# Optimization experiments

Hardware: AMD Instinct MI355X
Metric: run time of the kernel (lower is better)

Reference implementation:

```python
import jax, jax.numpy as jnp
import numpy as np

E = 64          # num_experts
TOPK = 8        # num_experts_per_tok
I = 512         # moe_intermediate_size
H = 1024        # hidden_size
G = 128         # awq group_size
T = 2048        # tokens (batch*seq)

# AWQ nibble unpack order: bit shifts [0,16,4,20,8,24,12,28] -> indices [0,4,1,5,2,6,3,7]
_AWQ_SHIFTS = jnp.array([0, 4, 1, 5, 2, 6, 3, 7], dtype=jnp.int32) * 4


def awq_dequant(qw, qz, scales, group_size=G):
    """qw: (K, N//8) int32, qz: (K//G, N//8) int32, scales: (K//G, N) float.
    Returns dense weight (K, N): (q - z) * scale with per-group zero/scale."""
    K = qw.shape[0]
    uq = ((qw[:, :, None] >> _AWQ_SHIFTS) & 0xF).reshape(K, -1)          # (K, N)
    uz = ((qz[:, :, None] >> _AWQ_SHIFTS) & 0xF).reshape(qz.shape[0], -1)  # (K//G, N)
    uz = jnp.repeat(uz, group_size, axis=0)                               # (K, N)
    sc = jnp.repeat(scales, group_size, axis=0)                           # (K, N)
    return (uq.astype(scales.dtype) - uz.astype(scales.dtype)) * sc


def setup_inputs() -> dict:
    key = jax.random.key(0)
    ks = jax.random.split(key, 8)
    imax = 2**31 - 1
    return {
        "x": jax.random.normal(ks[0], (T, H), dtype=jnp.float32),
        "gate_w": jax.random.normal(ks[1], (E, H), dtype=jnp.float32) * 0.02,
        "qweight1": jax.random.randint(ks[2], (H, (E * I) // 8), 0, imax, dtype=jnp.int32),
        "qzeros1": jax.random.randint(ks[3], (H // G, (E * I) // 8), 0, imax, dtype=jnp.int32),
        "scales1": jax.random.normal(ks[4], (H // G, E * I), dtype=jnp.float32) * 0.02,
        "qweight2": jax.random.randint(ks[5], (I, (E * H) // 8), 0, imax, dtype=jnp.int32),
        "qzeros2": jax.random.randint(ks[6], (I // G, (E * H) // 8), 0, imax, dtype=jnp.int32),
        "scales2": jax.random.normal(ks[7], (I // G, E * H), dtype=jnp.float32) * 0.02,
    }


def reference(x, gate_w, qweight1, qzeros1, scales1, qweight2, qzeros2, scales2):
    # dequant grouped expert weights
    w1 = awq_dequant(qweight1, qzeros1, scales1).T.reshape(E, I, H)   # (E, I, H)
    w2 = awq_dequant(qweight2, qzeros2, scales2).T.reshape(E, H, I)   # (E, H, I)

    # routing: softmax -> top-k -> renormalize
    logits = x @ gate_w.T                                             # (T, E)
    probs = jax.nn.softmax(logits, axis=-1)
    topv, topi = jax.lax.top_k(probs, TOPK)                           # (T, K)
    topv = topv / jnp.sum(topv, axis=-1, keepdims=True)
    cw = jnp.sum(jax.nn.one_hot(topi, E, dtype=x.dtype) * topv[..., None], axis=1)  # (T, E)

    # experts: out = sum_e cw[t,e] * silu(x @ w1[e].T) @ w2[e].T
    h = jax.nn.silu(jnp.einsum('th,eih->tei', x, w1))                 # (T, E, I)
    h = h * cw[:, :, None]                                            # fold combine weights
    out = jnp.einsum('tei,ehi->th', h, w2)                            # (T, H)
    return out
```

## Files before the change

kernel.cpp:

```cpp
#include <hip/hip_runtime.h>
#include <hip/hip_bf16.h>

#define T_TOK 2048
#define HID   1024
#define EXP   64
#define TOPK  8
#define IMED  512
#define N1 (EXP * IMED)
#define C1 (N1 / 8)
#define N2 (EXP * HID)
#define C2 (N2 / 8)

typedef __bf16 bf16x8 __attribute__((ext_vector_type(8)));
typedef float f32x4 __attribute__((ext_vector_type(4)));
typedef unsigned short ushortx8 __attribute__((ext_vector_type(8)));
typedef unsigned short ushortx4 __attribute__((ext_vector_type(4)));

__constant__ int kShifts[8] = {0, 16, 4, 20, 8, 24, 12, 28};

__device__ __forceinline__ void async16(const void* g, void* l) {
  __builtin_amdgcn_global_load_lds((const __attribute__((address_space(1))) void*)g,
                                   (__attribute__((address_space(3))) void*)l, 16, 0, 0);
}

__device__ __forceinline__ unsigned short f2bf(float f) {
  unsigned u = __builtin_bit_cast(unsigned, f);
  unsigned r = (u + 0x7fffu + ((u >> 16) & 1u)) >> 16;
  return (unsigned short)r;
}

__device__ __forceinline__ float bf2f(unsigned short b) {
  unsigned u = ((unsigned)b) << 16;
  return __builtin_bit_cast(float, u);
}

__device__ __forceinline__ bf16x8 unpack8(unsigned q, float s, float w) {
  bf16x8 r;
#pragma unroll
  for (int i = 0; i < 8; ++i) {
    const float qf = (float)((q >> (4 * i)) & 15u);
    r[i] = (__bf16)fmaf(qf, s, w);
  }
  return r;
}

__global__ __launch_bounds__(256) void routing_kernel(
    const float* __restrict__ x, const float* __restrict__ gate_w,
    int* __restrict__ counts, int* __restrict__ tok_list,
    int* __restrict__ hslot_list, float* __restrict__ cw_list,
    unsigned short* __restrict__ xbf) {
  const int t = blockIdx.x;
  const int tid = threadIdx.x;
  __shared__ float xs[HID];
  __shared__ float part[64][4];

  float4 v = reinterpret_cast<const float4*>(x + (size_t)t * HID)[tid];
  reinterpret_cast<float4*>(xs)[tid] = v;
  ushortx4 o;
  o[0] = f2bf(v.x); o[1] = f2bf(v.y); o[2] = f2bf(v.z); o[3] = f2bf(v.w);
  *reinterpret_cast<ushortx4*>(xbf + (size_t)t * HID + tid * 4) = o;
  __syncthreads();

  const int e = tid >> 2, seg = tid & 3;
  const float4* gp = reinterpret_cast<const float4*>(gate_w + (size_t)e * HID);
  const float4* xp = reinterpret_cast<const float4*>(xs);
  float acc = 0.f;
#pragma unroll 8
  for (int i = 0; i < 64; ++i) {
    float4 a = xp[i * 4 + seg];
    float4 b = gp[i * 4 + seg];
    acc = fmaf(a.x, b.x, acc);
    acc = fmaf(a.y, b.y, acc);
    acc = fmaf(a.z, b.z, acc);
    acc = fmaf(a.w, b.w, acc);
  }
  part[e][seg] = acc;
  __syncthreads();

  if (tid < 64) {
    float4 p = reinterpret_cast<const float4*>(part)[tid];
    float lg = (p.x + p.y) + (p.z + p.w);

    float m = lg;
    for (int off = 32; off; off >>= 1) m = fmaxf(m, __shfl_xor(m, off));
    float pe = expf(lg - m);
    float s = pe;
    for (int off = 32; off; off >>= 1) s += __shfl_xor(s, off);
    float prob = pe / s;

    float pcur = prob;
    float myv = 0.f;
    int myi = -1;
    float tsum = 0.f;
    for (int k = 0; k < TOPK; ++k) {
      float vv = pcur;
      int idx = tid;
      for (int off = 32; off; off >>= 1) {
        float ov = __shfl_xor(vv, off);
        int oi = __shfl_xor(idx, off);
        if (ov > vv || (ov == vv && oi < idx)) { vv = ov; idx = oi; }
      }
      tsum += vv;
      if (tid == k) { myv = vv; myi = idx; }
      if (tid == idx) pcur = -1.f;
    }

    if (tid < TOPK) {
      float cw = myv / tsum;
      int ex = myi;
      int slot = atomicAdd(&counts[ex], 1);
      tok_list[ex * T_TOK + slot] = t;
      hslot_list[ex * T_TOK + slot] = t * TOPK + tid;
      cw_list[ex * T_TOK + slot] = cw;
    }
  }
}

__global__ __launch_bounds__(256) void repack_kernel(
    const int* __restrict__ qw, unsigned* __restrict__ qk, int K, int C) {
  const int kd = blockIdx.y;
  const int c = blockIdx.x * 512 + threadIdx.x * 2;
  unsigned q[8][2];
#pragma unroll
  for (int r = 0; r < 8; ++r) {
    const int2 v = *reinterpret_cast<const int2*>(qw + (size_t)(kd * 8 + r) * C + c);
    q[r][0] = (unsigned)v.x;
    q[r][1] = (unsigned)v.y;
  }
  unsigned outd[16];
#pragma unroll
  for (int ci = 0; ci < 2; ++ci) {
#pragma unroll
    for (int jj = 0; jj < 8; ++jj) {
      const int sh = kShifts[jj];
      unsigned o = 0;
#pragma unroll
      for (int r = 0; r < 8; ++r) o |= ((q[r][ci] >> sh) & 0xFu) << (4 * r);
      outd[ci * 8 + jj] = o;
    }
  }
  unsigned* dst = qk + ((size_t)(c >> 1) * (K / 8) + kd) * 16;
#pragma unroll
  for (int i = 0; i < 4; ++i)
    *reinterpret_cast<uint4*>(dst + i * 4) = *reinterpret_cast<const uint4*>(&outd[i * 4]);
}

__global__ __launch_bounds__(256) void mfma_gemm1(
    const unsigned short* __restrict__ xbf, const unsigned* __restrict__ qk1,
    const int* __restrict__ qz1, const float* __restrict__ sc1,
    const int* __restrict__ counts, const int* __restrict__ tok_list,
    const int* __restrict__ hslot_list, const float* __restrict__ cw_list,
    unsigned short* __restrict__ h_buf) {
  const int e = blockIdx.z;
  const int n_e = counts[e];
  const int t0 = blockIdx.y * 64;
  if (t0 >= n_e) return;
  const int ntile = blockIdx.x;
  const int tid = threadIdx.x;
  const int wave = tid >> 6, lane = tid & 63;
  const int wm = wave & 1, wn = wave >> 1;
  const int fr = lane & 15, fq = lane >> 4;

  __shared__ unsigned short As[2][64 * 64];

  const int arow = tid >> 3;
  const int acb = ((tid & 7) ^ ((tid >> 3) & 7)) * 16;
  const int ta0 = tok_list[e * T_TOK + min(t0 + arow, n_e - 1)];
  const int ta1 = tok_list[e * T_TOK + min(t0 + 32 + arow, n_e - 1)];
  const char* ga0 = (const char*)(xbf + (size_t)ta0 * HID) + acb;
  const char* ga1 = (const char*)(xbf + (size_t)ta1 * HID) + acb;

  auto stage = [&](int b) {
    char* l = (char*)&As[b][0] + wave * 1024;
    async16(ga0, l);
    async16(ga1, l + 4096);
    ga0 += 128; ga1 += 128;
  };

  const int nbase = e * IMED + ntile * 64 + wn * 32;
  const unsigned* bl0 = qk1 + (size_t)(nbase >> 4) * 2048 + fq * 16 + fr;
  const unsigned* bl1 = bl0 + 2048;
  const int shz = ((fr >> 1) & 3) * 4 + (fr & 1) * 16;

  f32x4 acc[2][2];
#pragma unroll
  for (int i = 0; i < 2; ++i)
#pragma unroll
    for (int j = 0; j < 2; ++j) acc[i][j] = (f32x4){0.f, 0.f, 0.f, 0.f};

  stage(0);
  unsigned cb00 = bl0[0], cb01 = bl0[64], cb10 = bl1[0], cb11 = bl1[64];
  int p = 0;
#pragma unroll 1
  for (int g = 0; g < HID / 128; ++g) {
    const float s0f = sc1[(size_t)g * N1 + nbase + fr];
    const float s1f = sc1[(size_t)g * N1 + nbase + 16 + fr];
    const unsigned zd0 = (unsigned)qz1[(size_t)g * C1 + (nbase >> 3) + (fr >> 3)];
    const unsigned zd1 = (unsigned)qz1[(size_t)g * C1 + 2 + (nbase >> 3) + (fr >> 3)];
    const float w0f = -(float)((zd0 >> shz) & 15u) * s0f;
    const float w1f = -(float)((zd1 >> shz) & 15u) * s1f;
#pragma unroll
    for (int hh = 0; hh < 2; ++hh) {
      const int k0 = g * 128 + hh * 64;
      __syncthreads();
      if (k0 + 64 < HID) stage(p ^ 1);
      unsigned nb00 = 0, nb01 = 0, nb10 = 0, nb11 = 0;
      if (k0 + 64 < HID) {
        const unsigned* q0 = bl0 + (k0 + 64) * 2;
        const unsigned* q1 = bl1 + (k0 + 64) * 2;
        nb00 = q0[0]; nb01 = q0[64]; nb10 = q1[0]; nb11 = q1[64];
      }
      const bf16x8 b00 = unpack8(cb00, s0f, w0f);
      const bf16x8 b01 = unpack8(cb01, s0f, w0f);
      const bf16x8 b10 = unpack8(cb10, s1f, w1f);
      const bf16x8 b11 = unpack8(cb11, s1f, w1f);
#pragma unroll
      for (int kk = 0; kk < 2; ++kk) {
        bf16x8 af[2];
#pragma unroll
        for (int i = 0; i < 2; ++i) {
          const int row = wm * 32 + i * 16 + fr;
          af[i] = *reinterpret_cast<const bf16x8*>(
              &As[p][row * 64 + (((kk * 4 + fq) ^ (fr & 7)) * 8)]);
        }
        const bf16x8 b0 = kk ? b01 : b00;
        const bf16x8 b1 = kk ? b11 : b10;
        acc[0][0] = __builtin_amdgcn_mfma_f32_16x16x32_bf16(af[0], b0, acc[0][0], 0, 0, 0);
        acc[0][1] = __builtin_amdgcn_mfma_f32_16x16x32_bf16(af[0], b1, acc[0][1], 0, 0, 0);
        acc[1][0] = __builtin_amdgcn_mfma_f32_16x16x32_bf16(af[1], b0, acc[1][0], 0, 0, 0);
        acc[1][1] = __builtin_amdgcn_mfma_f32_16x16x32_bf16(af[1], b1, acc[1][1], 0, 0, 0);
      }
      cb00 = nb00; cb01 = nb01; cb10 = nb10; cb11 = nb11;
      p ^= 1;
    }
  }

#pragma unroll
  for (int i = 0; i < 2; ++i) {
#pragma unroll
    for (int r = 0; r < 4; ++r) {
      const int grow = t0 + wm * 32 + i * 16 + fq * 4 + r;
      if (grow < n_e) {
        const float cw = cw_list[e * T_TOK + grow];
        const int hs = hslot_list[e * T_TOK + grow];
        unsigned short* dst = h_buf + (size_t)hs * IMED + ntile * 64 + wn * 32 + fr;
#pragma unroll
        for (int j = 0; j < 2; ++j) {
          const float v = acc[i][j][r];
          dst[j * 16] = f2bf((v / (1.f + expf(-v))) * cw);
        }
      }
    }
  }
}

__global__ __launch_bounds__(256) void mfma_gemm2(
    const unsigned short* __restrict__ h_buf, const unsigned* __restrict__ qk2,
    const int* __restrict__ qz2, const float* __restrict__ sc2,
    const int* __restrict__ counts, const int* __restrict__ hslot_list,
    unsigned short* __restrict__ p_buf) {
  const int e = blockIdx.z;
  const int n_e = counts[e];
  const int t0 = blockIdx.y * 64;
  if (t0 >= n_e) return;
  const int ntile = blockIdx.x;
  const int tid = threadIdx.x;
  const int wave = tid >> 6, lane = tid & 63;
  const int wm = wave & 1, wn = wave >> 1;
  const int fr = lane & 15, fq = lane >> 4;

  __shared__ unsigned short As[2][64 * 64];

  const int arow = tid >> 3;
  const int acb = ((tid & 7) ^ ((tid >> 3) & 7)) * 16;
  const int ha0 = hslot_list[e * T_TOK + min(t0 + arow, n_e - 1)];
  const int ha1 = hslot_list[e * T_TOK + min(t0 + 32 + arow, n_e - 1)];
  const char* ga0 = (const char*)(h_buf + (size_t)ha0 * IMED) + acb;
  const char* ga1 = (const char*)(h_buf + (size_t)ha1 * IMED) + acb;

  auto stage = [&](int b) {
    char* l = (char*)&As[b][0] + wave * 1024;
    async16(ga0, l);
    async16(ga1, l + 4096);
    ga0 += 128; ga1 += 128;
  };

  const int nbase = e * HID + ntile * 64 + wn * 32;
  const unsigned* bl0 = qk2 + (size_t)(nbase >> 4) * 1024 + fq * 16 + fr;
  const unsigned* bl1 = bl0 + 1024;
  const int shz = ((fr >> 1) & 3) * 4 + (fr & 1) * 16;

  f32x4 acc[2][2];
#pragma unroll
  for (int i = 0; i < 2; ++i)
#pragma unroll
    for (int j = 0; j < 2; ++j) acc[i][j] = (f32x4){0.f, 0.f, 0.f, 0.f};

  stage(0);
  unsigned cb00 = bl0[0], cb01 = bl0[64], cb10 = bl1[0], cb11 = bl1[64];
  int p = 0;
#pragma unroll 1
  for (int g = 0; g < IMED / 128; ++g) {
    const float s0f = sc2[(size_t)g * N2 + nbase + fr];
    const float s1f = sc2[(size_t)g * N2 + nbase + 16 + fr];
    const unsigned zd0 = (unsigned)qz2[(size_t)g * C2 + (nbase >> 3) + (fr >> 3)];
    const unsigned zd1 = (unsigned)qz2[(size_t)g * C2 + 2 + (nbase >> 3) + (fr >> 3)];
    const float w0f = -(float)((zd0 >> shz) & 15u) * s0f;
    const float w1f = -(float)((zd1 >> shz) & 15u) * s1f;
#pragma unroll
    for (int hh = 0; hh < 2; ++hh) {
      const int k0 = g * 128 + hh * 64;
      __syncthreads();
      if (k0 + 64 < IMED) stage(p ^ 1);
      unsigned nb00 = 0, nb01 = 0, nb10 = 0, nb11 = 0;
      if (k0 + 64 < IMED) {
        const unsigned* q0 = bl0 + (k0 + 64) * 2;
        const unsigned* q1 = bl1 + (k0 + 64) * 2;
        nb00 = q0[0]; nb01 = q0[64]; nb10 = q1[0]; nb11 = q1[64];
      }
      const bf16x8 b00 = unpack8(cb00, s0f, w0f);
      const bf16x8 b01 = unpack8(cb01, s0f, w0f);
      const bf16x8 b10 = unpack8(cb10, s1f, w1f);
      const bf16x8 b11 = unpack8(cb11, s1f, w1f);
#pragma unroll
      for (int kk = 0; kk < 2; ++kk) {
        bf16x8 af[2];
#pragma unroll
        for (int i = 0; i < 2; ++i) {
          const int row = wm * 32 + i * 16 + fr;
          af[i] = *reinterpret_cast<const bf16x8*>(
              &As[p][row * 64 + (((kk * 4 + fq) ^ (fr & 7)) * 8)]);
        }
        const bf16x8 b0 = kk ? b01 : b00;
        const bf16x8 b1 = kk ? b11 : b10;
        acc[0][0] = __builtin_amdgcn_mfma_f32_16x16x32_bf16(af[0], b0, acc[0][0], 0, 0, 0);
        acc[0][1] = __builtin_amdgcn_mfma_f32_16x16x32_bf16(af[0], b1, acc[0][1], 0, 0, 0);
        acc[1][0] = __builtin_amdgcn_mfma_f32_16x16x32_bf16(af[1], b0, acc[1][0], 0, 0, 0);
        acc[1][1] = __builtin_amdgcn_mfma_f32_16x16x32_bf16(af[1], b1, acc[1][1], 0, 0, 0);
      }
      cb00 = nb00; cb01 = nb01; cb10 = nb10; cb11 = nb11;
      p ^= 1;
    }
  }

#pragma unroll
  for (int i = 0; i < 2; ++i) {
#pragma unroll
    for (int r = 0; r < 4; ++r) {
      const int grow = t0 + wm * 32 + i * 16 + fq * 4 + r;
      if (grow < n_e) {
        const int hs = hslot_list[e * T_TOK + grow];
        unsigned short* dst = p_buf + (size_t)hs * HID + ntile * 64 + wn * 32 + fr;
#pragma unroll
        for (int j = 0; j < 2; ++j) dst[j * 16] = f2bf(acc[i][j][r]);
      }
    }
  }
}

__global__ __launch_bounds__(256) void reduce_kernel(const unsigned short* __restrict__ p_buf,
                                                     float* __restrict__ out) {
  const int idx = blockIdx.x * 256 + threadIdx.x;
  const int t = idx >> 7;
  const int c0 = (idx & 127) * 8;
  float s[8] = {0.f, 0.f, 0.f, 0.f, 0.f, 0.f, 0.f, 0.f};
#pragma unroll
  for (int k = 0; k < TOPK; ++k) {
    ushortx8 v = *reinterpret_cast<const ushortx8*>(p_buf + ((size_t)t * TOPK + k) * HID + c0);
#pragma unroll
    for (int j = 0; j < 8; ++j) s[j] += bf2f(v[j]);
  }
  float* dst = out + (size_t)t * HID + c0;
  *reinterpret_cast<float4*>(dst) = make_float4(s[0], s[1], s[2], s[3]);
  *reinterpret_cast<float4*>(dst + 4) = make_float4(s[4], s[5], s[6], s[7]);
}

extern "C" void kernel_launch(void* const* d_in, const int* in_sizes, int n_in,
                              void* d_out, int out_size, void* d_ws, size_t ws_size,
                              hipStream_t stream) {
  const float* x      = (const float*)d_in[0];
  const float* gate_w = (const float*)d_in[1];
  const int*   qw1    = (const int*)d_in[2];
  const int*   qz1    = (const int*)d_in[3];
  const float* sc1    = (const float*)d_in[4];
  const int*   qw2    = (const int*)d_in[5];
  const int*   qz2    = (const int*)d_in[6];
  const float* sc2    = (const float*)d_in[7];
  float* out = (float*)d_out;

  char* ws = (char*)d_ws;
  int* counts           = (int*)(ws);
  int* tok_list         = (int*)(ws + 256);
  int* hslot_list       = (int*)(ws + 524544);
  float* cw_list        = (float*)(ws + 1048832);
  unsigned short* h_buf = (unsigned short*)(ws + 1573120);
  unsigned short* xbf   = (unsigned short*)(ws + 18350336);
  unsigned* qk1         = (unsigned*)(ws + 22544640);
  unsigned* qk2         = (unsigned*)(ws + 39321856);
  unsigned short* p_buf = (unsigned short*)(ws + 56099072);

  hipMemsetAsync(counts, 0, 256, stream);

  routing_kernel<<<T_TOK, 256, 0, stream>>>(x, gate_w, counts, tok_list, hslot_list, cw_list, xbf);
  repack_kernel<<<dim3(C1 / 512, HID / 8), 256, 0, stream>>>(qw1, qk1, HID, C1);
  repack_kernel<<<dim3(C2 / 512, IMED / 8), 256, 0, stream>>>(qw2, qk2, IMED, C2);

  mfma_gemm1<<<dim3(IMED / 64, T_TOK / 64, EXP), 256, 0, stream>>>(
      xbf, qk1, qz1, sc1, counts, tok_list, hslot_list, cw_list, h_buf);
  mfma_gemm2<<<dim3(HID / 64, T_TOK / 64, EXP), 256, 0, stream>>>(
      h_buf, qk2, qz2, sc2, counts, hslot_list, p_buf);
  reduce_kernel<<<(T_TOK * HID / 8) / 256, 256, 0, stream>>>(p_buf, out);
}
```

Measured before the change: 292.2 us.

## Switch expert GEMMs to fp16 with magic-number dequant and 16-column wave tiles

Converts activations, intermediate buffers and MFMA ops from bf16 to fp16, so int4 weights can be dequantized with the 0x6400 magic-number trick and packed half2 subtract/multiply instead of per-element float conversion and FMA. The repack kernel now writes a layout where each lane loads a contiguous uint2 per k-step. Each wave owns 16 output columns across all 64 rows instead of a 32x32 quadrant. Scale and zero loads are prefetched one group ahead. Fp16 has a narrower range than bf16, which risks overflow or precision differences, and the new wave tiling trades fewer dequant ops per wave for more LDS A-fragment reads.

```diff
diff --git a/kernel.cpp b/kernel.cpp
--- a/kernel.cpp
+++ b/kernel.cpp
@@ -11,10 +11,11 @@
 #define N2 (EXP * HID)
 #define C2 (N2 / 8)
 
-typedef __bf16 bf16x8 __attribute__((ext_vector_type(8)));
+typedef _Float16 h16x2 __attribute__((ext_vector_type(2)));
+typedef _Float16 h16x8 __attribute__((ext_vector_type(8)));
 typedef float f32x4 __attribute__((ext_vector_type(4)));
+typedef unsigned short ushortx4 __attribute__((ext_vector_type(4)));
 typedef unsigned short ushortx8 __attribute__((ext_vector_type(8)));
-typedef unsigned short ushortx4 __attribute__((ext_vector_type(4)));
 
 __constant__ int kShifts[8] = {0, 16, 4, 20, 8, 24, 12, 28};
 
@@ -23,32 +24,30 @@
                                    (__attribute__((address_space(3))) void*)l, 16, 0, 0);
 }
 
-__device__ __forceinline__ unsigned short f2bf(float f) {
-  unsigned u = __builtin_bit_cast(unsigned, f);
-  unsigned r = (u + 0x7fffu + ((u >> 16) & 1u)) >> 16;
-  return (unsigned short)r;
-}
-
-__device__ __forceinline__ float bf2f(unsigned short b) {
-  unsigned u = ((unsigned)b) << 16;
-  return __builtin_bit_cast(float, u);
-}
-
-__device__ __forceinline__ bf16x8 unpack8(unsigned q, float s, float w) {
-  bf16x8 r;
-#pragma unroll
-  for (int i = 0; i < 8; ++i) {
-    const float qf = (float)((q >> (4 * i)) & 15u);
-    r[i] = (__bf16)fmaf(qf, s, w);
-  }
-  return r;
+__device__ __forceinline__ unsigned short f2h(float f) {
+  return __builtin_bit_cast(unsigned short, (_Float16)f);
+}
+__device__ __forceinline__ float h2f(unsigned short b) {
+  return (float)__builtin_bit_cast(_Float16, b);
+}
+
+__device__ __forceinline__ h16x8 unpack8h(unsigned q, h16x2 sh2, h16x2 zh2) {
+  union { unsigned u[4]; h16x8 v; } out;
+#pragma unroll
+  for (int j = 0; j < 4; ++j) {
+    const unsigned m = ((q >> (4 * j)) & 0x000F000Fu) | 0x64006400u;
+    h16x2 d = __builtin_bit_cast(h16x2, m) - zh2;
+    d = d * sh2;
+    out.u[j] = __builtin_bit_cast(unsigned, d);
+  }
+  return out.v;
 }
 
 __global__ __launch_bounds__(256) void routing_kernel(
     const float* __restrict__ x, const float* __restrict__ gate_w,
     int* __restrict__ counts, int* __restrict__ tok_list,
     int* __restrict__ hslot_list, float* __restrict__ cw_list,
-    unsigned short* __restrict__ xbf) {
+    unsigned short* __restrict__ xh) {
   const int t = blockIdx.x;
   const int tid = threadIdx.x;
   __shared__ float xs[HID];
@@ -57,8 +56,8 @@
   float4 v = reinterpret_cast<const float4*>(x + (size_t)t * HID)[tid];
   reinterpret_cast<float4*>(xs)[tid] = v;
   ushortx4 o;
-  o[0] = f2bf(v.x); o[1] = f2bf(v.y); o[2] = f2bf(v.z); o[3] = f2bf(v.w);
-  *reinterpret_cast<ushortx4*>(xbf + (size_t)t * HID + tid * 4) = o;
+  o[0] = f2h(v.x); o[1] = f2h(v.y); o[2] = f2h(v.z); o[3] = f2h(v.w);
+  *reinterpret_cast<ushortx4*>(xh + (size_t)t * HID + tid * 4) = o;
   __syncthreads();
 
   const int e = tid >> 2, seg = tid & 3;
@@ -118,35 +117,40 @@
 
 __global__ __launch_bounds__(256) void repack_kernel(
     const int* __restrict__ qw, unsigned* __restrict__ qk, int K, int C) {
-  const int kd = blockIdx.y;
-  const int c = blockIdx.x * 512 + threadIdx.x * 2;
-  unsigned q[8][2];
+  const int pp = blockIdx.y;
+  const int t = pp >> 2, fq = pp & 3;
+  const int c2 = blockIdx.x * 512 + threadIdx.x * 2;
+  const int nblk = c2 >> 1;
+  unsigned o0[16], o1[16];
+#pragma unroll
+  for (int i = 0; i < 16; ++i) { o0[i] = 0u; o1[i] = 0u; }
+  const int k0a = t * 64 + fq * 8;
+  const int k0b = t * 64 + (fq + 4) * 8;
 #pragma unroll
   for (int r = 0; r < 8; ++r) {
-    const int2 v = *reinterpret_cast<const int2*>(qw + (size_t)(kd * 8 + r) * C + c);
-    q[r][0] = (unsigned)v.x;
-    q[r][1] = (unsigned)v.y;
-  }
-  unsigned outd[16];
-#pragma unroll
-  for (int ci = 0; ci < 2; ++ci) {
-#pragma unroll
-    for (int jj = 0; jj < 8; ++jj) {
-      const int sh = kShifts[jj];
-      unsigned o = 0;
-#pragma unroll
-      for (int r = 0; r < 8; ++r) o |= ((q[r][ci] >> sh) & 0xFu) << (4 * r);
-      outd[ci * 8 + jj] = o;
-    }
-  }
-  unsigned* dst = qk + ((size_t)(c >> 1) * (K / 8) + kd) * 16;
-#pragma unroll
-  for (int i = 0; i < 4; ++i)
-    *reinterpret_cast<uint4*>(dst + i * 4) = *reinterpret_cast<const uint4*>(&outd[i * 4]);
+    const int2 va = *reinterpret_cast<const int2*>(qw + (size_t)(k0a + r) * C + c2);
+    const int2 vb = *reinterpret_cast<const int2*>(qw + (size_t)(k0b + r) * C + c2);
+    const int outsh = (r & 1) * 16 + (r >> 1) * 4;
+    const unsigned qa[2] = {(unsigned)va.x, (unsigned)va.y};
+    const unsigned qb[2] = {(unsigned)vb.x, (unsigned)vb.y};
+#pragma unroll
+    for (int ci = 0; ci < 2; ++ci) {
+#pragma unroll
+      for (int j = 0; j < 8; ++j) {
+        const int sh = kShifts[j];
+        o0[ci * 8 + j] |= ((qa[ci] >> sh) & 0xFu) << outsh;
+        o1[ci * 8 + j] |= ((qb[ci] >> sh) & 0xFu) << outsh;
+      }
+    }
+  }
+  unsigned* dst = qk + (size_t)nblk * 2 * K + t * 128 + fq * 32;
+#pragma unroll
+  for (int idx = 0; idx < 16; ++idx)
+    *reinterpret_cast<uint2*>(dst + idx * 2) = make_uint2(o0[idx], o1[idx]);
 }
 
 __global__ __launch_bounds__(256) void mfma_gemm1(
-    const unsigned short* __restrict__ xbf, const unsigned* __restrict__ qk1,
+    const unsigned short* __restrict__ xh, const unsigned* __restrict__ qk1,
     const int* __restrict__ qz1, const float* __restrict__ sc1,
     const int* __restrict__ counts, const int* __restrict__ tok_list,
     const int* __restrict__ hslot_list, const float* __restrict__ cw_list,
@@ -158,7 +162,6 @@
   const int ntile = blockIdx.x;
   const int tid = threadIdx.x;
   const int wave = tid >> 6, lane = tid & 63;
-  const int wm = wave & 1, wn = wave >> 1;
   const int fr = lane & 15, fq = lane >> 4;
 
   __shared__ unsigned short As[2][64 * 64];
@@ -167,8 +170,8 @@
   const int acb = ((tid & 7) ^ ((tid >> 3) & 7)) * 16;
   const int ta0 = tok_list[e * T_TOK + min(t0 + arow, n_e - 1)];
   const int ta1 = tok_list[e * T_TOK + min(t0 + 32 + arow, n_e - 1)];
-  const char* ga0 = (const char*)(xbf + (size_t)ta0 * HID) + acb;
-  const char* ga1 = (const char*)(xbf + (size_t)ta1 * HID) + acb;
+  const char* ga0 = (const char*)(xh + (size_t)ta0 * HID) + acb;
+  const char* ga1 = (const char*)(xh + (size_t)ta1 * HID) + acb;
 
   auto stage = [&](int b) {
     char* l = (char*)&As[b][0] + wave * 1024;
@@ -177,78 +180,67 @@
     ga0 += 128; ga1 += 128;
   };
 
-  const int nbase = e * IMED + ntile * 64 + wn * 32;
-  const unsigned* bl0 = qk1 + (size_t)(nbase >> 4) * 2048 + fq * 16 + fr;
-  const unsigned* bl1 = bl0 + 2048;
+  const int nbase = e * IMED + ntile * 64 + wave * 16;
+  const unsigned* bp = qk1 + (size_t)(nbase >> 4) * (2 * HID) + fq * 32 + fr * 2;
+  const int col = nbase + fr;
   const int shz = ((fr >> 1) & 3) * 4 + (fr & 1) * 16;
 
-  f32x4 acc[2][2];
-#pragma unroll
-  for (int i = 0; i < 2; ++i)
-#pragma unroll
-    for (int j = 0; j < 2; ++j) acc[i][j] = (f32x4){0.f, 0.f, 0.f, 0.f};
+  f32x4 acc[4];
+#pragma unroll
+  for (int i = 0; i < 4; ++i) acc[i] = (f32x4){0.f, 0.f, 0.f, 0.f};
 
   stage(0);
-  unsigned cb00 = bl0[0], cb01 = bl0[64], cb10 = bl1[0], cb11 = bl1[64];
+  uint2 qcur = *reinterpret_cast<const uint2*>(bp);
+  float s_cur = sc1[col];
+  unsigned zd_cur = (unsigned)qz1[col >> 3];
   int p = 0;
 #pragma unroll 1
   for (int g = 0; g < HID / 128; ++g) {
-    const float s0f = sc1[(size_t)g * N1 + nbase + fr];
-    const float s1f = sc1[(size_t)g * N1 + nbase + 16 + fr];
-    const unsigned zd0 = (unsigned)qz1[(size_t)g * C1 + (nbase >> 3) + (fr >> 3)];
-    const unsigned zd1 = (unsigned)qz1[(size_t)g * C1 + 2 + (nbase >> 3) + (fr >> 3)];
-    const float w0f = -(float)((zd0 >> shz) & 15u) * s0f;
-    const float w1f = -(float)((zd1 >> shz) & 15u) * s1f;
+    const unsigned shb = (unsigned)f2h(s_cur);
+    const h16x2 sh2 = __builtin_bit_cast(h16x2, shb | (shb << 16));
+    const unsigned zb = 0x6400u | ((zd_cur >> shz) & 15u);
+    const h16x2 zh2 = __builtin_bit_cast(h16x2, zb | (zb << 16));
+    float s_nxt = 0.f; unsigned zd_nxt = 0u;
 #pragma unroll
     for (int hh = 0; hh < 2; ++hh) {
-      const int k0 = g * 128 + hh * 64;
+      const int t = g * 2 + hh;
       __syncthreads();
-      if (k0 + 64 < HID) stage(p ^ 1);
-      unsigned nb00 = 0, nb01 = 0, nb10 = 0, nb11 = 0;
-      if (k0 + 64 < HID) {
-        const unsigned* q0 = bl0 + (k0 + 64) * 2;
-        const unsigned* q1 = bl1 + (k0 + 64) * 2;
-        nb00 = q0[0]; nb01 = q0[64]; nb10 = q1[0]; nb11 = q1[64];
-      }
-      const bf16x8 b00 = unpack8(cb00, s0f, w0f);
-      const bf16x8 b01 = unpack8(cb01, s0f, w0f);
-      const bf16x8 b10 = unpack8(cb10, s1f, w1f);
-      const bf16x8 b11 = unpack8(cb11, s1f, w1f);
+      if (t + 1 < HID / 64) stage(p ^ 1);
+      uint2 qnext = make_uint2(0u, 0u);
+      if (t + 1 < HID / 64) qnext = *reinterpret_cast<const uint2*>(bp + (t + 1) * 128);
+      if (hh == 1 && g + 1 < HID / 128) {
+        s_nxt = sc1[(size_t)(g + 1) * N1 + col];
+        zd_nxt = (unsigned)qz1[(size_t)(g + 1) * C1 + (col >> 3)];
+      }
+      const h16x8 b0 = unpack8h(qcur.x, sh2, zh2);
+      const h16x8 b1 = unpack8h(qcur.y, sh2, zh2);
 #pragma unroll
       for (int kk = 0; kk < 2; ++kk) {
-        bf16x8 af[2];
-#pragma unroll
-        for (int i = 0; i < 2; ++i) {
-          const int row = wm * 32 + i * 16 + fr;
-          af[i] = *reinterpret_cast<const bf16x8*>(
+        const h16x8 bb = kk ? b1 : b0;
+#pragma unroll
+        for (int i = 0; i < 4; ++i) {
+          const int row = i * 16 + fr;
+          const h16x8 a = *reinterpret_cast<const h16x8*>(
               &As[p][row * 64 + (((kk * 4 + fq) ^ (fr & 7)) * 8)]);
+          acc[i] = __builtin_amdgcn_mfma_f32_16x16x32_f16(a, bb, acc[i], 0, 0, 0);
         }
-        const bf16x8 b0 = kk ? b01 : b00;
-        const bf16x8 b1 = kk ? b11 : b10;
-        acc[0][0] = __builtin_amdgcn_mfma_f32_16x16x32_bf16(af[0], b0, acc[0][0], 0, 0, 0);
-        acc[0][1] = __builtin_amdgcn_mfma_f32_16x16x32_bf16(af[0], b1, acc[0][1], 0, 0, 0);
-        acc[1][0] = __builtin_amdgcn_mfma_f32_16x16x32_bf16(af[1], b0, acc[1][0], 0, 0, 0);
-        acc[1][1] = __builtin_amdgcn_mfma_f32_16x16x32_bf16(af[1], b1, acc[1][1], 0, 0, 0);
-      }
-      cb00 = nb00; cb01 = nb01; cb10 = nb10; cb11 = nb11;
-      p ^= 1;
-    }
-  }
-
-#pragma unroll
-  for (int i = 0; i < 2; ++i) {
+      }
+      qcur = qnext; p ^= 1;
+    }
+    s_cur = s_nxt; zd_cur = zd_nxt;
+  }
+
+#pragma unroll
+  for (int i = 0; i < 4; ++i) {
 #pragma unroll
     for (int r = 0; r < 4; ++r) {
-      const int grow = t0 + wm * 32 + i * 16 + fq * 4 + r;
+      const int grow = t0 + i * 16 + fq * 4 + r;
       if (grow < n_e) {
         const float cw = cw_list[e * T_TOK + grow];
         const int hs = hslot_list[e * T_TOK + grow];
-        unsigned short* dst = h_buf + (size_t)hs * IMED + ntile * 64 + wn * 32 + fr;
-#pragma unroll
-        for (int j = 0; j < 2; ++j) {
-          const float v = acc[i][j][r];
-          dst[j * 16] = f2bf((v / (1.f + expf(-v))) * cw);
-        }
+        const float v = acc[i][r];
+        h_buf[(size_t)hs * IMED + ntile * 64 + wave * 16 + fr] =
+            f2h((v / (1.f + expf(-v))) * cw);
       }
     }
   }
@@ -266,7 +258,6 @@
   const int ntile = blockIdx.x;
   const int tid = threadIdx.x;
   const int wave = tid >> 6, lane = tid & 63;
-  const int wm = wave & 1, wn = wave >> 1;
   const int fr = lane & 15, fq = lane >> 4;
 
   __shared__ unsigned short As[2][64 * 64];
@@ -285,74 +276,64 @@
     ga0 += 128; ga1 += 128;
   };
 
-  const int nbase = e * HID + ntile * 64 + wn * 32;
-  const unsigned* bl0 = qk2 + (size_t)(nbase >> 4) * 1024 + fq * 16 + fr;
-  const unsigned* bl1 = bl0 + 1024;
+  const int nbase = e * HID + ntile * 64 + wave * 16;
+  const unsigned* bp = qk2 + (size_t)(nbase >> 4) * (2 * IMED) + fq * 32 + fr * 2;
+  const int col = nbase + fr;
   const int shz = ((fr >> 1) & 3) * 4 + (fr & 1) * 16;
 
-  f32x4 acc[2][2];
-#pragma unroll
-  for (int i = 0; i < 2; ++i)
-#pragma unroll
-    for (int j = 0; j < 2; ++j) acc[i][j] = (f32x4){0.f, 0.f, 0.f, 0.f};
+  f32x4 acc[4];
+#pragma unroll
+  for (int i = 0; i < 4; ++i) acc[i] = (f32x4){0.f, 0.f, 0.f, 0.f};
 
   stage(0);
-  unsigned cb00 = bl0[0], cb01 = bl0[64], cb10 = bl1[0], cb11 = bl1[64];
+  uint2 qcur = *reinterpret_cast<const uint2*>(bp);
+  float s_cur = sc2[col];
+  unsigned zd_cur = (unsigned)qz2[col >> 3];
   int p = 0;
 #pragma unroll 1
   for (int g = 0; g < IMED / 128; ++g) {
-    const float s0f = sc2[(size_t)g * N2 + nbase + fr];
-    const float s1f = sc2[(size_t)g * N2 + nbase + 16 + fr];
-    const unsigned zd0 = (unsigned)qz2[(size_t)g * C2 + (nbase >> 3) + (fr >> 3)];
-    const unsigned zd1 = (unsigned)qz2[(size_t)g * C2 + 2 + (nbase >> 3) + (fr >> 3)];
-    const float w0f = -(float)((zd0 >> shz) & 15u) * s0f;
-    const float w1f = -(float)((zd1 >> shz) & 15u) * s1f;
+    const unsigned shb = (unsigned)f2h(s_cur);
+    const h16x2 sh2 = __builtin_bit_cast(h16x2, shb | (shb << 16));
+    const unsigned zb = 0x6400u | ((zd_cur >> shz) & 15u);
+    const h16x2 zh2 = __builtin_bit_cast(h16x2, zb | (zb << 16));
+    float s_nxt = 0.f; unsigned zd_nxt = 0u;
 #pragma unroll
     for (int hh = 0; hh < 2; ++hh) {
-      const int k0 = g * 128 + hh * 64;
+      const int t = g * 2 + hh;
       __syncthreads();
-      if (k0 + 64 < IMED) stage(p ^ 1);
-      unsigned nb00 = 0, nb01 = 0, nb10 = 0, nb11 = 0;
-      if (k0 + 64 < IMED) {
-        const unsigned* q0 = bl0 + (k0 + 64) * 2;
-        const unsigned* q1 = bl1 + (k0 + 64) * 2;
-        nb00 = q0[0]; nb01 = q0[64]; nb10 = q1[0]; nb11 = q1[64];
-      }
-      const bf16x8 b00 = unpack8(cb00, s0f, w0f);
-      const bf16x8 b01 = unpack8(cb01, s0f, w0f);
-      const bf16x8 b10 = unpack8(cb10, s1f, w1f);
-      const bf16x8 b11 = unpack8(cb11, s1f, w1f);
+      if (t + 1 < IMED / 64) stage(p ^ 1);
+      uint2 qnext = make_uint2(0u, 0u);
+      if (t + 1 < IMED / 64) qnext = *reinterpret_cast<const uint2*>(bp + (t + 1) * 128);
+      if (hh == 1 && g + 1 < IMED / 128) {
+        s_nxt = sc2[(size_t)(g + 1) * N2 + col];
+        zd_nxt = (unsigned)qz2[(size_t)(g + 1) * C2 + (col >> 3)];
+      }
+      const h16x8 b0 = unpack8h(qcur.x, sh2, zh2);
+      const h16x8 b1 = unpack8h(qcur.y, sh2, zh2);
 #pragma unroll
       for (int kk = 0; kk < 2; ++kk) {
-        bf16x8 af[2];
-#pragma unroll
-        for (int i = 0; i < 2; ++i) {
-          const int row = wm * 32 + i * 16 + fr;
-          af[i] = *reinterpret_cast<const bf16x8*>(
+        const h16x8 bb = kk ? b1 : b0;
+#pragma unroll
+        for (int i = 0; i < 4; ++i) {
+          const int row = i * 16 + fr;
+          const h16x8 a = *reinterpret_cast<const h16x8*>(
               &As[p][row * 64 + (((kk * 4 + fq) ^ (fr & 7)) * 8)]);
+          acc[i] = __builtin_amdgcn_mfma_f32_16x16x32_f16(a, bb, acc[i], 0, 0, 0);
         }
-        const bf16x8 b0 = kk ? b01 : b00;
-        const bf16x8 b1 = kk ? b11 : b10;
-        acc[0][0] = __builtin_amdgcn_mfma_f32_16x16x32_bf16(af[0], b0, acc[0][0], 0, 0, 0);
-        acc[0][1] = __builtin_amdgcn_mfma_f32_16x16x32_bf16(af[0], b1, acc[0][1], 0, 0, 0);
-        acc[1][0] = __builtin_amdgcn_mfma_f32_16x16x32_bf16(af[1], b0, acc[1][0], 0, 0, 0);
-        acc[1][1] = __builtin_amdgcn_mfma_f32_16x16x32_bf16(af[1], b1, acc[1][1], 0, 0, 0);
-      }
-      cb00 = nb00; cb01 = nb01; cb10 = nb10; cb11 = nb11;
-      p ^= 1;
-    }
-  }
-
-#pragma unroll
-  for (int i = 0; i < 2; ++i) {
+      }
+      qcur = qnext; p ^= 1;
+    }
+    s_cur = s_nxt; zd_cur = zd_nxt;
+  }
+
+#pragma unroll
+  for (int i = 0; i < 4; ++i) {
 #pragma unroll
     for (int r = 0; r < 4; ++r) {
-      const int grow = t0 + wm * 32 + i * 16 + fq * 4 + r;
+      const int grow = t0 + i * 16 + fq * 4 + r;
       if (grow < n_e) {
         const int hs = hslot_list[e * T_TOK + grow];
-        unsigned short* dst = p_buf + (size_t)hs * HID + ntile * 64 + wn * 32 + fr;
-#pragma unroll
-        for (int j = 0; j < 2; ++j) dst[j * 16] = f2bf(acc[i][j][r]);
+        p_buf[(size_t)hs * HID + ntile * 64 + wave * 16 + fr] = f2h(acc[i][r]);
       }
     }
   }
@@ -368,7 +349,7 @@
   for (int k = 0; k < TOPK; ++k) {
     ushortx8 v = *reinterpret_cast<const ushortx8*>(p_buf + ((size_t)t * TOPK + k) * HID + c0);
 #pragma unroll
-    for (int j = 0; j < 8; ++j) s[j] += bf2f(v[j]);
+    for (int j = 0; j < 8; ++j) s[j] += h2f(v[j]);
   }
   float* dst = out + (size_t)t * HID + c0;
   *reinterpret_cast<float4*>(dst) = make_float4(s[0], s[1], s[2], s[3]);
@@ -394,19 +375,19 @@
   int* hslot_list       = (int*)(ws + 524544);
   float* cw_list        = (float*)(ws + 1048832);
   unsigned short* h_buf = (unsigned short*)(ws + 1573120);
-  unsigned short* xbf   = (unsigned short*)(ws + 18350336);
+  unsigned short* xh    = (unsigned short*)(ws + 18350336);
   unsigned* qk1         = (unsigned*)(ws + 22544640);
   unsigned* qk2         = (unsigned*)(ws + 39321856);
   unsigned short* p_buf = (unsigned short*)(ws + 56099072);
 
   hipMemsetAsync(counts, 0, 256, stream);
 
-  routing_kernel<<<T_TOK, 256, 0, stream>>>(x, gate_w, counts, tok_list, hslot_list, cw_list, xbf);
-  repack_kernel<<<dim3(C1 / 512, HID / 8), 256, 0, stream>>>(qw1, qk1, HID, C1);
-  repack_kernel<<<dim3(C2 / 512, IMED / 8), 256, 0, stream>>>(qw2, qk2, IMED, C2);
+  routing_kernel<<<T_TOK, 256, 0, stream>>>(x, gate_w, counts, tok_list, hslot_list, cw_list, xh);
+  repack_kernel<<<dim3(C1 / 512, HID / 16), 256, 0, stream>>>(qw1, qk1, HID, C1);
+  repack_kernel<<<dim3(C2 / 512, IMED / 16), 256, 0, stream>>>(qw2, qk2, IMED, C2);
 
   mfma_gemm1<<<dim3(IMED / 64, T_TOK / 64, EXP), 256, 0, stream>>>(
-      xbf, qk1, qz1, sc1, counts, tok_list, hslot_list, cw_list, h_buf);
+      xh, qk1, qz1, sc1, counts, tok_list, hslot_list, cw_list, h_buf);
   mfma_gemm2<<<dim3(HID / 64, T_TOK / 64, EXP), 256, 0, stream>>>(
       h_buf, qk2, qz2, sc2, counts, hslot_list, p_buf);
   reduce_kernel<<<(T_TOK * HID / 8) / 256, 256, 0, stream>>>(p_buf, out);
```

After: 265.5 us. -9.1%, faster.
